# Performance work log

Hardware: AMD Instinct MI355X
Metric: run time of the kernel (lower is better)

The kernel has to match this reference:

```python
import jax, jax.numpy as jnp
import numpy as np

HEADS = 8
DIM_HEAD = 32
EPS = 1e-5


def _rel_index(h, w):
    # matches Attention._generate_relative_index (static, computed on host)
    coords = np.stack(np.meshgrid(np.arange(h), np.arange(w), indexing='ij')).reshape(2, -1)
    rel = coords[:, :, None] - coords[:, None, :]  # [2, n, n]
    rel[0] += h - 1
    rel[1] += w - 1
    rel[0] *= 2 * w - 1
    idx = rel.sum(0).reshape(-1)
    # torch.clamp(relative_index, 0, max_index) -- indices are already in range here
    return jnp.asarray(np.clip(idx, 0, (2 * h - 1) * (2 * w - 1) - 1))


def _layernorm(x, g, b):
    m = jnp.mean(x, axis=-1, keepdims=True)
    v = jnp.var(x, axis=-1, keepdims=True)
    return (x - m) * jax.lax.rsqrt(v + EPS) * g + b


def setup_inputs() -> dict:
    key = jax.random.key(0)
    ks = jax.random.split(key, 6)
    B, C, H, W = 64, 384, 16, 16
    inner = HEADS * DIM_HEAD  # 256
    hid = 4 * C               # 1536
    def nrm(k, shape, s=0.02):
        return jax.random.normal(k, shape, jnp.float32) * s
    return {
        'x': jax.random.normal(ks[0], (B, C, H, W), jnp.float32),
        'ln1_g': jnp.ones((C,), jnp.float32),
        'ln1_b': jnp.zeros((C,), jnp.float32),
        'w_qkv': nrm(ks[1], (C, 3 * inner)),
        'bias_table': nrm(ks[2], ((2 * H - 1) * (2 * W - 1), HEADS)),
        'w_out': nrm(ks[3], (inner, C)),
        'b_out': jnp.zeros((C,), jnp.float32),
        'ln2_g': jnp.ones((C,), jnp.float32),
        'ln2_b': jnp.zeros((C,), jnp.float32),
        'w_ff1': nrm(ks[4], (C, hid)),
        'b_ff1': jnp.zeros((hid,), jnp.float32),
        'w_ff2': nrm(ks[5], (hid, C)),
        'b_ff2': jnp.zeros((C,), jnp.float32),
    }


def reference(x, ln1_g, ln1_b, w_qkv, bias_table, w_out, b_out,
              ln2_g, ln2_b, w_ff1, b_ff1, w_ff2, b_ff2):
    B, C, H, W = x.shape
    n = H * W
    t = x.reshape(B, C, n).transpose(0, 2, 1)  # [B, n, C]

    # --- attention branch (PreNorm(LayerNorm) -> Attention) ---
    a = _layernorm(t, ln1_g, ln1_b)
    qkv = a @ w_qkv  # [B, n, 3*inner]
    q, k, v = jnp.split(qkv, 3, axis=-1)
    def split_heads(z):
        return z.reshape(B, n, HEADS, DIM_HEAD).transpose(0, 2, 1, 3)  # [B, h, n, d]
    q, k, v = split_heads(q), split_heads(k), split_heads(v)
    dots = jnp.einsum('bhid,bhjd->bhij', q, k) * (DIM_HEAD ** -0.5)
    idx = _rel_index(H, W)  # [n*n]
    rel_bias = bias_table[idx].reshape(n, n, HEADS).transpose(2, 0, 1)[None]  # [1, h, n, n]
    attn = jax.nn.softmax(dots + rel_bias, axis=-1)
    o = jnp.einsum('bhij,bhjd->bhid', attn, v)
    o = o.transpose(0, 2, 1, 3).reshape(B, n, HEADS * DIM_HEAD)
    attn_out = o @ w_out + b_out  # to_out Linear (dropout=0)

    # --- feedforward branch (PreNorm(LayerNorm) -> FFN) ---
    f = _layernorm(t, ln2_g, ln2_b)
    f = jax.nn.gelu(f @ w_ff1 + b_ff1, approximate=False) @ w_ff2 + b_ff2

    y = t + attn_out + f  # x_adjusted + attn_out + ff_out
    return y.transpose(0, 2, 1).reshape(B, C, H, W)
```

## Files before the change

### kernel.cpp

```cpp
#include <hip/hip_runtime.h>

typedef __bf16 bf16;
typedef __bf16 bf16x8 __attribute__((ext_vector_type(8)));
typedef float f32x4 __attribute__((ext_vector_type(4)));

__device__ __forceinline__ void gll16(const void* g, void* l) {
    __builtin_amdgcn_global_load_lds((const __attribute__((address_space(1))) void*)g,
                                     (__attribute__((address_space(3))) void*)l, 16, 0, 0);
}

#define WBAR(N) asm volatile("s_waitcnt vmcnt(" #N ")\n\ts_barrier" ::: "memory")

__device__ __forceinline__ float gelu_f(float v) {
    float x2 = v * v;
    float sn = v * fmaf(-0.0713540072f, x2, -1.5957691216f);
    float e  = __expf(sn);
    return v * __builtin_amdgcn_rcpf(1.0f + e);
}

__launch_bounds__(256)
__global__ void prep_kernel(const float* __restrict__ wqkv, const float* __restrict__ wout,
                            const float* __restrict__ wff1, const float* __restrict__ wff2,
                            bf16* __restrict__ wqkvT, bf16* __restrict__ woutT,
                            bf16* __restrict__ wff1T, bf16* __restrict__ wff2T,
                            const float* __restrict__ x,
                            const float* __restrict__ g1, const float* __restrict__ b1,
                            const float* __restrict__ g2, const float* __restrict__ b2,
                            bf16* __restrict__ a, bf16* __restrict__ f) {
    __shared__ __align__(16) float smem[12672 + 512 + 64];
    const int tid = threadIdx.x;
    int g = blockIdx.x;
    if (g < 1536) {
        float (*tl)[33] = (float (*)[33])smem;
        const float* in; bf16* out; int R, Cc, bx, by;
        if (g < 288)       { in = wqkv; out = wqkvT; R = 384;  Cc = 768;  bx = g % 24; by = g / 24; }
        else if (g < 384)  { g -= 288; in = wout; out = woutT; R = 256;  Cc = 384;  bx = g % 12; by = g / 12; }
        else if (g < 960)  { g -= 384; in = wff1; out = wff1T; R = 384;  Cc = 1536; bx = g % 48; by = g / 48; }
        else               { g -= 960; in = wff2; out = wff2T; R = 1536; Cc = 384;  bx = g % 12; by = g / 12; }
        const int c0 = bx * 32, r0 = by * 32;
        const int cl = tid & 31, r8 = tid >> 5;
#pragma unroll
        for (int k = 0; k < 4; k++) {
            int r = k * 8 + r8;
            tl[r][cl] = in[(size_t)(r0 + r) * Cc + c0 + cl];
        }
        __syncthreads();
#pragma unroll
        for (int k = 0; k < 4; k++) {
            int cc = k * 8 + r8;
            out[(size_t)(c0 + cc) * R + r0 + cl] = (bf16)tl[cl][cc];
        }
        return;
    }
    g -= 1536;
    float (*tile)[33] = (float (*)[33])smem;
    float (*S)[32]  = (float (*)[32])(smem + 12672);
    float (*SS)[32] = (float (*)[32])(smem + 12928);
    float* Mn = smem + 13184;
    float* Rs = smem + 13216;
    const int bb = g >> 3;
    const int i0 = (g & 7) * 32;
    {
        const int i_l = tid & 31, c_l = tid >> 5;
        const size_t base = (size_t)bb * 384 * 256 + i0 + i_l;
#pragma unroll 6
        for (int c = c_l; c < 384; c += 8)
            tile[c][i_l] = x[base + (size_t)c * 256];
    }
    __syncthreads();
    {
        const int i_s = tid & 31, p = tid >> 5;
        float s = 0.f, ss = 0.f;
#pragma unroll 6
        for (int j = 0; j < 48; j++) {
            float v = tile[p * 48 + j][i_s];
            s += v; ss += v * v;
        }
        S[p][i_s] = s; SS[p][i_s] = ss;
    }
    __syncthreads();
    if (tid < 32) {
        float t1 = 0.f, t2 = 0.f;
#pragma unroll
        for (int p = 0; p < 8; p++) { t1 += S[p][tid]; t2 += SS[p][tid]; }
        float mean = t1 * (1.0f / 384.0f);
        float var  = t2 * (1.0f / 384.0f) - mean * mean;
        Mn[tid] = mean;
        Rs[tid] = rsqrtf(var + 1e-5f);
    }
    __syncthreads();
    const int lane = tid & 63, w = tid >> 6;
#pragma unroll
    for (int rr = 0; rr < 8; rr++) {
        const int i = w * 8 + rr;
        const float mean = Mn[i], rstd = Rs[i];
        const size_t orow = ((size_t)bb * 256 + i0 + i) * 384;
#pragma unroll
        for (int pass = 0; pass < 6; pass++) {
            const int c = pass * 64 + lane;
            float nh = (tile[c][i] - mean) * rstd;
            a[orow + c] = (bf16)(nh * g1[c] + b1[c]);
            f[orow + c] = (bf16)(nh * g2[c] + b2[c]);
        }
    }
}

#define STAGE128(buf, kb)                                                   \
    {                                                                       \
        bf16* sA = lds + (buf) * 8192;                                      \
        bf16* sB = sA + 4096;                                               \
        gll16(Abase + (size_t)r0 * K + (kb) + ksw, sA + c0 * 8);            \
        gll16(Abase + (size_t)r1 * K + (kb) + ksw, sA + c1 * 8);            \
        gll16(Bbase + (size_t)r0 * K + (kb) + ksw, sB + c0 * 8);            \
        gll16(Bbase + (size_t)r1 * K + (kb) + ksw, sB + c1 * 8);            \
    }
#define COMPUTE128(buf)                                                     \
    {                                                                       \
        const bf16* sA = lds + (buf) * 8192;                                \
        const bf16* sB = sA + 4096;                                         \
        bf16x8 af[4], bfr[4];                                               \
        _Pragma("unroll") for (int i = 0; i < 4; i++)                       \
            af[i] = *(const bf16x8*)(sA + (wm + i * 16 + l16) * 32 + rsw);  \
        _Pragma("unroll") for (int j = 0; j < 4; j++)                       \
            bfr[j] = *(const bf16x8*)(sB + (wn + j * 16 + l16) * 32 + rsw); \
        _Pragma("unroll") for (int i = 0; i < 4; i++)                       \
            _Pragma("unroll") for (int j = 0; j < 4; j++)                   \
                acc[i][j] = __builtin_amdgcn_mfma_f32_16x16x32_bf16(af[i], bfr[j], acc[i][j], 0, 0, 0); \
    }
#define GEMM128_PRO_KLOOP(BID)                                                       \
    const int x_ = ((BID) >> 3) % nx;                                                \
    const int y_ = ((BID) & 7) + 8 * ((BID) / (8 * nx));                             \
    const int m0 = y_ * 128, n0 = x_ * 128;                                          \
    const int lane = tid & 63, w = tid >> 6;                                         \
    const int l16 = lane & 15, quad = lane >> 4;                                     \
    const int wm = (w & 1) * 64, wn = (w >> 1) * 64;                                 \
    f32x4 zero = {0.f, 0.f, 0.f, 0.f};                                               \
    f32x4 acc[4][4];                                                                 \
    _Pragma("unroll") for (int i = 0; i < 4; i++)                                    \
        _Pragma("unroll") for (int j = 0; j < 4; j++) acc[i][j] = zero;              \
    const int c0 = tid, c1 = tid + 256;                                              \
    const int r0 = c0 >> 2, r1 = c1 >> 2;                                            \
    const int ksw = (((tid & 3) ^ ((tid >> 3) & 3)) * 8);                            \
    const int rsw = ((quad ^ ((l16 >> 1) & 3)) * 8);                                 \
    const bf16* Abase = A + (size_t)m0 * K;                                          \
    const bf16* Bbase = Bt + (size_t)n0 * K;                                         \
    STAGE128(0, 0);                                                                  \
    STAGE128(1, 32);                                                                 \
    const int nt = K >> 5;                                                           \
    int t = 0;                                                                       \
    for (; t < nt - 2; ++t) {                                                        \
        WBAR(4);                                                                     \
        STAGE128((t + 2) % 3, (t + 2) * 32);                                         \
        COMPUTE128(t % 3);                                                           \
    }                                                                                \
    WBAR(4); COMPUTE128(t % 3); ++t;                                                 \
    WBAR(0); COMPUTE128(t % 3);                                                      \
    __syncthreads();

template <int EPI>
__launch_bounds__(256)
__global__ void gemm_bt(const bf16* __restrict__ A, const bf16* __restrict__ Bt,
                        const float* __restrict__ bias, bf16* __restrict__ C,
                        int M, int N, int K, int nx) {
    __shared__ __align__(16) bf16 lds[24576];
    const int tid = threadIdx.x;
    GEMM128_PRO_KLOOP(blockIdx.x)
#pragma unroll
    for (int j = 0; j < 4; j++) {
        const int col = wn + j * 16 + l16;
        float bv = 0.f;
        if (EPI >= 1) bv = bias[n0 + col];
#pragma unroll
        for (int i = 0; i < 4; i++) {
            const int row0 = wm + i * 16 + quad * 4;
#pragma unroll
            for (int r = 0; r < 4; r++) {
                float v = acc[i][j][r] + bv;
                if (EPI == 2) v = gelu_f(v);
                lds[(row0 + r) * 128 + col] = (bf16)v;
            }
        }
    }
    __syncthreads();
#pragma unroll
    for (int it = 0; it < 8; it++) {
        const int ch = tid + it * 256;
        const int row = ch >> 4, cc = (ch & 15) * 8;
        *(bf16x8*)(C + (size_t)(m0 + row) * N + n0 + cc) = *(const bf16x8*)(lds + row * 128 + cc);
    }
}

__launch_bounds__(256)
__global__ void stage3_kernel(const bf16* __restrict__ A, const bf16* __restrict__ Bt,
                              const float* __restrict__ bias, bf16* __restrict__ C,
                              const bf16* __restrict__ qkv, const float* __restrict__ btab,
                              bf16* __restrict__ o) {
    __shared__ __align__(16) char smem[70928];
    const int tid = threadIdx.x;
    const int gg = blockIdx.x;
    if (gg & 3) {
        const int bid = (gg >> 2) * 3 + (gg & 3) - 1;
        bf16* lds = (bf16*)smem;
        const int K = 384, N = 1536, nx = 12;
        GEMM128_PRO_KLOOP(bid)
#pragma unroll
        for (int j = 0; j < 4; j++) {
            const int col = wn + j * 16 + l16;
            const float bv = bias[n0 + col];
#pragma unroll
            for (int i = 0; i < 4; i++) {
                const int row0 = wm + i * 16 + quad * 4;
#pragma unroll
                for (int r = 0; r < 4; r++) {
                    float v = gelu_f(acc[i][j][r] + bv);
                    lds[(row0 + r) * 128 + col] = (bf16)v;
                }
            }
        }
        __syncthreads();
#pragma unroll
        for (int it = 0; it < 8; it++) {
            const int ch = tid + it * 256;
            const int row = ch >> 4, cc = (ch & 15) * 8;
            *(bf16x8*)(C + (size_t)(m0 + row) * N + n0 + cc) = *(const bf16x8*)(lds + row * 128 + cc);
        }
        return;
    }
    const int aid = gg >> 2;
    float* sbias = (float*)smem;
    bf16* sK = (bf16*)(smem + 3856);
    bf16 (*sVt)[264] = (bf16 (*)[264])(smem + 20240);
    bf16 (*sP)[16][264] = (bf16 (*)[16][264])(smem + 37136);
    const int h  = (aid >> 3) & 7;
    const int bb = (aid & 7) + 8 * (aid >> 6);
    const int lane = tid & 63, w = tid >> 6;
    const int l16 = lane & 15, quad = lane >> 4;
    const int rsw = ((quad ^ ((l16 >> 1) & 3)) * 8);
    const size_t qkvb = (size_t)bb * 256 * 768;
    const bf16* Qbase = qkv + qkvb + h * 32;
    const bf16* Kbase = qkv + qkvb + 256 + h * 32;
    const bf16* Vbase = qkv + qkvb + 512 + h * 32;

    for (int e = tid; e < 961; e += 256) sbias[e] = btab[e * 8 + h];
#pragma unroll
    for (int it = 0; it < 4; it++) {
        const int ch = it * 256 + tid;
        const int row = ch >> 2;
        const int d8 = (((ch & 3) ^ ((ch >> 3) & 3)) * 8);
        gll16(Kbase + (size_t)row * 768 + d8, sK + ch * 8);
    }
#pragma unroll
    for (int it = 0; it < 4; it++) {
        const int ch = it * 256 + tid;
        const int k = ch >> 2, d8 = (ch & 3) * 8;
        bf16x8 vv = *(const bf16x8*)(Vbase + (size_t)k * 768 + d8);
#pragma unroll
        for (int j = 0; j < 8; j++)
            sVt[d8 + j][k] = vv[j];
    }
    __syncthreads();

    f32x4 zero = {0.f, 0.f, 0.f, 0.f};
    for (int qc = 0; qc < 4; qc++) {
        const int qbase = qc * 64 + w * 16;
        bf16x8 qf = *(const bf16x8*)(Qbase + (size_t)(qbase + l16) * 768 + quad * 8);
        f32x4 s[16];
#pragma unroll
        for (int kt = 0; kt < 16; kt++) {
            bf16x8 kf = *(const bf16x8*)(sK + (kt * 16 + l16) * 32 + rsw);
            s[kt] = __builtin_amdgcn_mfma_f32_16x16x32_bf16(qf, kf, zero, 0, 0, 0);
        }
        const int qi0 = qbase + quad * 4;
        float mx[4] = {-1e30f, -1e30f, -1e30f, -1e30f};
#pragma unroll
        for (int kt = 0; kt < 16; kt++) {
            const int j = kt * 16 + l16;
            const int yj = j >> 4, xj = j & 15;
#pragma unroll
            for (int r = 0; r < 4; r++) {
                const int q = qi0 + r;
                const int tix = ((q >> 4) - yj + 15) * 31 + ((q & 15) - xj + 15);
                float v = s[kt][r] * 0.17677669529663687f + sbias[tix];
                s[kt][r] = v;
                mx[r] = fmaxf(mx[r], v);
            }
        }
#pragma unroll
        for (int r = 0; r < 4; r++)
            for (int msk = 1; msk < 16; msk <<= 1)
                mx[r] = fmaxf(mx[r], __shfl_xor(mx[r], msk, 64));
        float sum[4] = {0.f, 0.f, 0.f, 0.f};
#pragma unroll
        for (int kt = 0; kt < 16; kt++)
#pragma unroll
            for (int r = 0; r < 4; r++) {
                float e = __expf(s[kt][r] - mx[r]);
                s[kt][r] = e;
                sum[r] += e;
            }
#pragma unroll
        for (int r = 0; r < 4; r++) {
            for (int msk = 1; msk < 16; msk <<= 1)
                sum[r] += __shfl_xor(sum[r], msk, 64);
            sum[r] = 1.0f / sum[r];
        }
#pragma unroll
        for (int kt = 0; kt < 16; kt++)
#pragma unroll
            for (int r = 0; r < 4; r++)
                sP[w][quad * 4 + r][kt * 16 + l16] = (bf16)(s[kt][r] * sum[r]);
        f32x4 oacc[2];
        oacc[0] = zero; oacc[1] = zero;
#pragma unroll
        for (int ks = 0; ks < 8; ks++) {
            bf16x8 pf = *(const bf16x8*)(&sP[w][l16][ks * 32 + quad * 8]);
#pragma unroll
            for (int dt = 0; dt < 2; dt++) {
                bf16x8 vf = *(const bf16x8*)(&sVt[dt * 16 + l16][ks * 32 + quad * 8]);
                oacc[dt] = __builtin_amdgcn_mfma_f32_16x16x32_bf16(pf, vf, oacc[dt], 0, 0, 0);
            }
        }
#pragma unroll
        for (int dt = 0; dt < 2; dt++)
#pragma unroll
            for (int r = 0; r < 4; r++)
                o[(size_t)(bb * 256 + qbase + quad * 4 + r) * 256 + h * 32 + dt * 16 + l16] = (bf16)oacc[dt][r];
    }
}

__launch_bounds__(256)
__global__ void fin_dual(const bf16* __restrict__ Af, const bf16* __restrict__ Bf,
                         const bf16* __restrict__ Ao, const bf16* __restrict__ Bo,
                         const float* __restrict__ bff2, const float* __restrict__ bout,
                         const float* __restrict__ xres, float* __restrict__ out, int nx) {
    __shared__ __align__(16) bf16 lds[24576];
    const int tid = threadIdx.x;
    const int g = blockIdx.x;
    const int x_ = (g >> 3) % nx;
    const int y_ = (g & 7) + 8 * (g / (8 * nx));
    const int m0 = y_ * 128, n0 = x_ * 128;
    const int lane = tid & 63, w = tid >> 6;
    const int l16 = lane & 15, quad = lane >> 4;
    const int wm = (w & 1) * 64, wn = (w >> 1) * 64;
    f32x4 acc[4][4];
    { f32x4 z = {0.f, 0.f, 0.f, 0.f};
#pragma unroll
      for (int i = 0; i < 4; i++)
#pragma unroll
          for (int j = 0; j < 4; j++) acc[i][j] = z; }
    const int c0 = tid, c1 = tid + 256;
    const int r0 = c0 >> 2, r1 = c1 >> 2;
    const int ksw = (((tid & 3) ^ ((tid >> 3) & 3)) * 8);
    const int rsw = ((quad ^ ((l16 >> 1) & 3)) * 8);
    const bf16* A1 = Af + (size_t)m0 * 1536;
    const bf16* B1 = Bf + (size_t)n0 * 1536;
    const bf16* A2 = Ao + (size_t)m0 * 256;
    const bf16* B2 = Bo + (size_t)n0 * 256;

#define STGD(buf, s)                                                                \
    {   bf16* sA = lds + (buf) * 8192;                                              \
        bf16* sB = sA + 4096;                                                       \
        if ((s) < 48) {                                                             \
            const int kb = (s) * 32;                                                \
            gll16(A1 + (size_t)r0 * 1536 + kb + ksw, sA + c0 * 8);                  \
            gll16(A1 + (size_t)r1 * 1536 + kb + ksw, sA + c1 * 8);                  \
            gll16(B1 + (size_t)r0 * 1536 + kb + ksw, sB + c0 * 8);                  \
            gll16(B1 + (size_t)r1 * 1536 + kb + ksw, sB + c1 * 8);                  \
        } else {                                                                    \
            const int kb = ((s) - 48) * 32;                                         \
            gll16(A2 + (size_t)r0 * 256 + kb + ksw, sA + c0 * 8);                   \
            gll16(A2 + (size_t)r1 * 256 + kb + ksw, sA + c1 * 8);                   \
            gll16(B2 + (size_t)r0 * 256 + kb + ksw, sB + c0 * 8);                   \
            gll16(B2 + (size_t)r1 * 256 + kb + ksw, sB + c1 * 8);                   \
        } }

    STGD(0, 0); STGD(1, 1);
    int s = 0;
    for (; s < 54; ++s) {
        WBAR(4);
        STGD((s + 2) % 3, s + 2);
        COMPUTE128(s % 3);
    }
    WBAR(4); COMPUTE128(s % 3); ++s;
    WBAR(0); COMPUTE128(s % 3);
    __syncthreads();
#undef STGD

#pragma unroll
    for (int j = 0; j < 4; j++) {
        const int col = wn + j * 16 + l16;
        const float bv = bff2[n0 + col] + bout[n0 + col];
#pragma unroll
        for (int i = 0; i < 4; i++) {
            const int row0 = wm + i * 16 + quad * 4;
#pragma unroll
            for (int r = 0; r < 4; r++)
                lds[col * 132 + row0 + r] = (bf16)(acc[i][j][r] + bv);
        }
    }
    __syncthreads();
    const int b = m0 >> 8, ib = m0 & 255;
#pragma unroll
    for (int it = 0; it < 8; it++) {
        const int ch = tid + it * 256;
        const int cl = ch >> 4, ic = (ch & 15) * 8;
        const size_t base = (size_t)(b * 384 + n0 + cl) * 256 + ib + ic;
        bf16x8 ff = *(const bf16x8*)(lds + cl * 132 + ic);
        const f32x4* xr = (const f32x4*)(xres + base);
        f32x4 o0, o1;
#pragma unroll
        for (int e = 0; e < 4; e++) o0[e] = xr[0][e] + (float)ff[e];
#pragma unroll
        for (int e = 0; e < 4; e++) o1[e] = xr[1][e] + (float)ff[e + 4];
        ((f32x4*)(out + base))[0] = o0;
        ((f32x4*)(out + base))[1] = o1;
    }
}

extern "C" void kernel_launch(void* const* d_in, const int* in_sizes, int n_in,
                              void* d_out, int out_size, void* d_ws, size_t ws_size,
                              hipStream_t stream) {
    const float* x    = (const float*)d_in[0];
    const float* g1   = (const float*)d_in[1];
    const float* b1   = (const float*)d_in[2];
    const float* wqkv = (const float*)d_in[3];
    const float* btab = (const float*)d_in[4];
    const float* wout = (const float*)d_in[5];
    const float* bout = (const float*)d_in[6];
    const float* g2   = (const float*)d_in[7];
    const float* b2   = (const float*)d_in[8];
    const float* wff1 = (const float*)d_in[9];
    const float* bff1 = (const float*)d_in[10];
    const float* wff2 = (const float*)d_in[11];
    const float* bff2 = (const float*)d_in[12];
    float* out = (float*)d_out;

    bf16* ws = (bf16*)d_ws;
    const size_t NA = 6291456;
    bf16* wqkvT   = ws;
    bf16* woutT   = wqkvT + 294912;
    bf16* wff1T   = woutT + 98304;
    bf16* wff2T   = wff1T + 589824;
    bf16* f_buf   = ws + 1572864;
    bf16* a_buf   = f_buf + NA;
    bf16* qkv_buf = a_buf + NA;
    bf16* o_buf   = qkv_buf + 12582912;
    bf16* ffh_buf = o_buf + 4194304;

    dim3 b256(256);
    prep_kernel<<<2048, b256, 0, stream>>>(wqkv, wout, wff1, wff2, wqkvT, woutT, wff1T, wff2T,
                                           x, g1, b1, g2, b2, a_buf, f_buf);
    gemm_bt<0><<<6 * 128, b256, 0, stream>>>(a_buf, wqkvT, nullptr, qkv_buf, 16384, 768, 384, 6);
    stage3_kernel<<<2048, b256, 0, stream>>>(f_buf, wff1T, bff1, ffh_buf, qkv_buf, btab, o_buf);
    fin_dual<<<3 * 128, b256, 0, stream>>>(ffh_buf, wff2T, o_buf, woutT, bff2, bout, x, out, 3);
}
```

Baseline: 235.4 us.

## Split fused attention/FF1 kernel and use 128x256 GEMM tiles

Replaces the combined stage3 kernel, which interleaved attention blocks with FF1 GEMM blocks, with a standalone attention kernel followed by a separate FF1 GEMM launch. Both the QKV and FF1 GEMMs move to a new 128x256 tile kernel with 8 N-subtiles per wave, for more reuse of each A tile per K step. The change cuts block counts and raises the per-thread register and LDS footprint, which can lower occupancy. It also gives up the overlap of attention and GEMM work that the fused launch had.

```diff
diff --git a/kernel.cpp b/kernel.cpp
--- a/kernel.cpp
+++ b/kernel.cpp
@@ -105,15 +105,95 @@
     }
 }
 
-#define STAGE128(buf, kb)                                                   \
+#define STAGEW(buf, kb)                                                     \
     {                                                                       \
-        bf16* sA = lds + (buf) * 8192;                                      \
+        bf16* sA = lds + (buf) * 12288;                                     \
         bf16* sB = sA + 4096;                                               \
-        gll16(Abase + (size_t)r0 * K + (kb) + ksw, sA + c0 * 8);            \
-        gll16(Abase + (size_t)r1 * K + (kb) + ksw, sA + c1 * 8);            \
-        gll16(Bbase + (size_t)r0 * K + (kb) + ksw, sB + c0 * 8);            \
-        gll16(Bbase + (size_t)r1 * K + (kb) + ksw, sB + c1 * 8);            \
-    }
+        gll16(Abase + (size_t)rS * K + (kb) + ksw, sA + tid * 8);           \
+        gll16(Abase + (size_t)(rS + 64) * K + (kb) + ksw, sA + (tid + 256) * 8); \
+        gll16(Bbase + (size_t)rS * K + (kb) + ksw, sB + tid * 8);           \
+        gll16(Bbase + (size_t)(rS + 64) * K + (kb) + ksw, sB + (tid + 256) * 8); \
+        gll16(Bbase + (size_t)(rS + 128) * K + (kb) + ksw, sB + (tid + 512) * 8); \
+        gll16(Bbase + (size_t)(rS + 192) * K + (kb) + ksw, sB + (tid + 768) * 8); \
+    }
+#define COMPUTEW(buf)                                                       \
+    {                                                                       \
+        const bf16* sA = lds + (buf) * 12288;                               \
+        const bf16* sB = sA + 4096;                                         \
+        bf16x8 af[4], bfr[8];                                               \
+        _Pragma("unroll") for (int i = 0; i < 4; i++)                       \
+            af[i] = *(const bf16x8*)(sA + (wm + i * 16 + l16) * 32 + rsw);  \
+        _Pragma("unroll") for (int j = 0; j < 8; j++)                       \
+            bfr[j] = *(const bf16x8*)(sB + (wn + j * 16 + l16) * 32 + rsw); \
+        _Pragma("unroll") for (int i = 0; i < 4; i++)                       \
+            _Pragma("unroll") for (int j = 0; j < 8; j++)                   \
+                acc[i][j] = __builtin_amdgcn_mfma_f32_16x16x32_bf16(af[i], bfr[j], acc[i][j], 0, 0, 0); \
+    }
+
+template <int EPI>
+__launch_bounds__(256)
+__global__ void gemm_w(const bf16* __restrict__ A, const bf16* __restrict__ Bt,
+                       const float* __restrict__ bias, bf16* __restrict__ C,
+                       int M, int N, int K, int nx) {
+    __shared__ __align__(16) bf16 lds[36864];
+    const int tid = threadIdx.x;
+    const int g = blockIdx.x;
+    const int x_ = (g >> 3) % nx;
+    const int y_ = (g & 7) + 8 * (g / (8 * nx));
+    const int m0 = y_ * 128, n0 = x_ * 256;
+    const int lane = tid & 63, w = tid >> 6;
+    const int l16 = lane & 15, quad = lane >> 4;
+    const int wm = (w & 1) * 64, wn = (w >> 1) * 128;
+    f32x4 acc[4][8];
+    { f32x4 z = {0.f, 0.f, 0.f, 0.f};
+#pragma unroll
+      for (int i = 0; i < 4; i++)
+#pragma unroll
+          for (int j = 0; j < 8; j++) acc[i][j] = z; }
+    const int rS = tid >> 2;
+    const int ksw = (((tid & 3) ^ ((tid >> 3) & 3)) * 8);
+    const int rsw = ((quad ^ ((l16 >> 1) & 3)) * 8);
+    const bf16* Abase = A + (size_t)m0 * K;
+    const bf16* Bbase = Bt + (size_t)n0 * K;
+
+    STAGEW(0, 0);
+    STAGEW(1, 32);
+    const int nt = K >> 5;
+    int t = 0;
+    for (; t < nt - 2; ++t) {
+        WBAR(6);
+        STAGEW((t + 2) % 3, (t + 2) * 32);
+        COMPUTEW(t % 3);
+    }
+    WBAR(6); COMPUTEW(t % 3); ++t;
+    WBAR(0); COMPUTEW(t % 3);
+    __syncthreads();
+
+#pragma unroll
+    for (int j = 0; j < 8; j++) {
+        const int col = wn + j * 16 + l16;
+        float bv = 0.f;
+        if (EPI >= 1) bv = bias[n0 + col];
+#pragma unroll
+        for (int i = 0; i < 4; i++) {
+            const int row0 = wm + i * 16 + quad * 4;
+#pragma unroll
+            for (int r = 0; r < 4; r++) {
+                float v = acc[i][j][r] + bv;
+                if (EPI == 2) v = gelu_f(v);
+                lds[(row0 + r) * 256 + col] = (bf16)v;
+            }
+        }
+    }
+    __syncthreads();
+#pragma unroll
+    for (int it = 0; it < 16; it++) {
+        const int ch = tid + it * 256;
+        const int row = ch >> 5, cc = (ch & 31) * 8;
+        *(bf16x8*)(C + (size_t)(m0 + row) * N + n0 + cc) = *(const bf16x8*)(lds + row * 256 + cc);
+    }
+}
+
 #define COMPUTE128(buf)                                                     \
     {                                                                       \
         const bf16* sA = lds + (buf) * 8192;                                \
@@ -127,206 +207,6 @@
             _Pragma("unroll") for (int j = 0; j < 4; j++)                   \
                 acc[i][j] = __builtin_amdgcn_mfma_f32_16x16x32_bf16(af[i], bfr[j], acc[i][j], 0, 0, 0); \
     }
-#define GEMM128_PRO_KLOOP(BID)                                                       \
-    const int x_ = ((BID) >> 3) % nx;                                                \
-    const int y_ = ((BID) & 7) + 8 * ((BID) / (8 * nx));                             \
-    const int m0 = y_ * 128, n0 = x_ * 128;                                          \
-    const int lane = tid & 63, w = tid >> 6;                                         \
-    const int l16 = lane & 15, quad = lane >> 4;                                     \
-    const int wm = (w & 1) * 64, wn = (w >> 1) * 64;                                 \
-    f32x4 zero = {0.f, 0.f, 0.f, 0.f};                                               \
-    f32x4 acc[4][4];                                                                 \
-    _Pragma("unroll") for (int i = 0; i < 4; i++)                                    \
-        _Pragma("unroll") for (int j = 0; j < 4; j++) acc[i][j] = zero;              \
-    const int c0 = tid, c1 = tid + 256;                                              \
-    const int r0 = c0 >> 2, r1 = c1 >> 2;                                            \
-    const int ksw = (((tid & 3) ^ ((tid >> 3) & 3)) * 8);                            \
-    const int rsw = ((quad ^ ((l16 >> 1) & 3)) * 8);                                 \
-    const bf16* Abase = A + (size_t)m0 * K;                                          \
-    const bf16* Bbase = Bt + (size_t)n0 * K;                                         \
-    STAGE128(0, 0);                                                                  \
-    STAGE128(1, 32);                                                                 \
-    const int nt = K >> 5;                                                           \
-    int t = 0;                                                                       \
-    for (; t < nt - 2; ++t) {                                                        \
-        WBAR(4);                                                                     \
-        STAGE128((t + 2) % 3, (t + 2) * 32);                                         \
-        COMPUTE128(t % 3);                                                           \
-    }                                                                                \
-    WBAR(4); COMPUTE128(t % 3); ++t;                                                 \
-    WBAR(0); COMPUTE128(t % 3);                                                      \
-    __syncthreads();
-
-template <int EPI>
-__launch_bounds__(256)
-__global__ void gemm_bt(const bf16* __restrict__ A, const bf16* __restrict__ Bt,
-                        const float* __restrict__ bias, bf16* __restrict__ C,
-                        int M, int N, int K, int nx) {
-    __shared__ __align__(16) bf16 lds[24576];
-    const int tid = threadIdx.x;
-    GEMM128_PRO_KLOOP(blockIdx.x)
-#pragma unroll
-    for (int j = 0; j < 4; j++) {
-        const int col = wn + j * 16 + l16;
-        float bv = 0.f;
-        if (EPI >= 1) bv = bias[n0 + col];
-#pragma unroll
-        for (int i = 0; i < 4; i++) {
-            const int row0 = wm + i * 16 + quad * 4;
-#pragma unroll
-            for (int r = 0; r < 4; r++) {
-                float v = acc[i][j][r] + bv;
-                if (EPI == 2) v = gelu_f(v);
-                lds[(row0 + r) * 128 + col] = (bf16)v;
-            }
-        }
-    }
-    __syncthreads();
-#pragma unroll
-    for (int it = 0; it < 8; it++) {
-        const int ch = tid + it * 256;
-        const int row = ch >> 4, cc = (ch & 15) * 8;
-        *(bf16x8*)(C + (size_t)(m0 + row) * N + n0 + cc) = *(const bf16x8*)(lds + row * 128 + cc);
-    }
-}
-
-__launch_bounds__(256)
-__global__ void stage3_kernel(const bf16* __restrict__ A, const bf16* __restrict__ Bt,
-                              const float* __restrict__ bias, bf16* __restrict__ C,
-                              const bf16* __restrict__ qkv, const float* __restrict__ btab,
-                              bf16* __restrict__ o) {
-    __shared__ __align__(16) char smem[70928];
-    const int tid = threadIdx.x;
-    const int gg = blockIdx.x;
-    if (gg & 3) {
-        const int bid = (gg >> 2) * 3 + (gg & 3) - 1;
-        bf16* lds = (bf16*)smem;
-        const int K = 384, N = 1536, nx = 12;
-        GEMM128_PRO_KLOOP(bid)
-#pragma unroll
-        for (int j = 0; j < 4; j++) {
-            const int col = wn + j * 16 + l16;
-            const float bv = bias[n0 + col];
-#pragma unroll
-            for (int i = 0; i < 4; i++) {
-                const int row0 = wm + i * 16 + quad * 4;
-#pragma unroll
-                for (int r = 0; r < 4; r++) {
-                    float v = gelu_f(acc[i][j][r] + bv);
-                    lds[(row0 + r) * 128 + col] = (bf16)v;
-                }
-            }
-        }
-        __syncthreads();
-#pragma unroll
-        for (int it = 0; it < 8; it++) {
-            const int ch = tid + it * 256;
-            const int row = ch >> 4, cc = (ch & 15) * 8;
-            *(bf16x8*)(C + (size_t)(m0 + row) * N + n0 + cc) = *(const bf16x8*)(lds + row * 128 + cc);
-        }
-        return;
-    }
-    const int aid = gg >> 2;
-    float* sbias = (float*)smem;
-    bf16* sK = (bf16*)(smem + 3856);
-    bf16 (*sVt)[264] = (bf16 (*)[264])(smem + 20240);
-    bf16 (*sP)[16][264] = (bf16 (*)[16][264])(smem + 37136);
-    const int h  = (aid >> 3) & 7;
-    const int bb = (aid & 7) + 8 * (aid >> 6);
-    const int lane = tid & 63, w = tid >> 6;
-    const int l16 = lane & 15, quad = lane >> 4;
-    const int rsw = ((quad ^ ((l16 >> 1) & 3)) * 8);
-    const size_t qkvb = (size_t)bb * 256 * 768;
-    const bf16* Qbase = qkv + qkvb + h * 32;
-    const bf16* Kbase = qkv + qkvb + 256 + h * 32;
-    const bf16* Vbase = qkv + qkvb + 512 + h * 32;
-
-    for (int e = tid; e < 961; e += 256) sbias[e] = btab[e * 8 + h];
-#pragma unroll
-    for (int it = 0; it < 4; it++) {
-        const int ch = it * 256 + tid;
-        const int row = ch >> 2;
-        const int d8 = (((ch & 3) ^ ((ch >> 3) & 3)) * 8);
-        gll16(Kbase + (size_t)row * 768 + d8, sK + ch * 8);
-    }
-#pragma unroll
-    for (int it = 0; it < 4; it++) {
-        const int ch = it * 256 + tid;
-        const int k = ch >> 2, d8 = (ch & 3) * 8;
-        bf16x8 vv = *(const bf16x8*)(Vbase + (size_t)k * 768 + d8);
-#pragma unroll
-        for (int j = 0; j < 8; j++)
-            sVt[d8 + j][k] = vv[j];
-    }
-    __syncthreads();
-
-    f32x4 zero = {0.f, 0.f, 0.f, 0.f};
-    for (int qc = 0; qc < 4; qc++) {
-        const int qbase = qc * 64 + w * 16;
-        bf16x8 qf = *(const bf16x8*)(Qbase + (size_t)(qbase + l16) * 768 + quad * 8);
-        f32x4 s[16];
-#pragma unroll
-        for (int kt = 0; kt < 16; kt++) {
-            bf16x8 kf = *(const bf16x8*)(sK + (kt * 16 + l16) * 32 + rsw);
-            s[kt] = __builtin_amdgcn_mfma_f32_16x16x32_bf16(qf, kf, zero, 0, 0, 0);
-        }
-        const int qi0 = qbase + quad * 4;
-        float mx[4] = {-1e30f, -1e30f, -1e30f, -1e30f};
-#pragma unroll
-        for (int kt = 0; kt < 16; kt++) {
-            const int j = kt * 16 + l16;
-            const int yj = j >> 4, xj = j & 15;
-#pragma unroll
-            for (int r = 0; r < 4; r++) {
-                const int q = qi0 + r;
-                const int tix = ((q >> 4) - yj + 15) * 31 + ((q & 15) - xj + 15);
-                float v = s[kt][r] * 0.17677669529663687f + sbias[tix];
-                s[kt][r] = v;
-                mx[r] = fmaxf(mx[r], v);
-            }
-        }
-#pragma unroll
-        for (int r = 0; r < 4; r++)
-            for (int msk = 1; msk < 16; msk <<= 1)
-                mx[r] = fmaxf(mx[r], __shfl_xor(mx[r], msk, 64));
-        float sum[4] = {0.f, 0.f, 0.f, 0.f};
-#pragma unroll
-        for (int kt = 0; kt < 16; kt++)
-#pragma unroll
-            for (int r = 0; r < 4; r++) {
-                float e = __expf(s[kt][r] - mx[r]);
-                s[kt][r] = e;
-                sum[r] += e;
-            }
-#pragma unroll
-        for (int r = 0; r < 4; r++) {
-            for (int msk = 1; msk < 16; msk <<= 1)
-                sum[r] += __shfl_xor(sum[r], msk, 64);
-            sum[r] = 1.0f / sum[r];
-        }
-#pragma unroll
-        for (int kt = 0; kt < 16; kt++)
-#pragma unroll
-            for (int r = 0; r < 4; r++)
-                sP[w][quad * 4 + r][kt * 16 + l16] = (bf16)(s[kt][r] * sum[r]);
-        f32x4 oacc[2];
-        oacc[0] = zero; oacc[1] = zero;
-#pragma unroll
-        for (int ks = 0; ks < 8; ks++) {
-            bf16x8 pf = *(const bf16x8*)(&sP[w][l16][ks * 32 + quad * 8]);
-#pragma unroll
-            for (int dt = 0; dt < 2; dt++) {
-                bf16x8 vf = *(const bf16x8*)(&sVt[dt * 16 + l16][ks * 32 + quad * 8]);
-                oacc[dt] = __builtin_amdgcn_mfma_f32_16x16x32_bf16(pf, vf, oacc[dt], 0, 0, 0);
-            }
-        }
-#pragma unroll
-        for (int dt = 0; dt < 2; dt++)
-#pragma unroll
-            for (int r = 0; r < 4; r++)
-                o[(size_t)(bb * 256 + qbase + quad * 4 + r) * 256 + h * 32 + dt * 16 + l16] = (bf16)oacc[dt][r];
-    }
-}
 
 __launch_bounds__(256)
 __global__ void fin_dual(const bf16* __restrict__ Af, const bf16* __restrict__ Bf,
@@ -414,6 +294,113 @@
         for (int e = 0; e < 4; e++) o1[e] = xr[1][e] + (float)ff[e + 4];
         ((f32x4*)(out + base))[0] = o0;
         ((f32x4*)(out + base))[1] = o1;
+    }
+}
+
+__launch_bounds__(256)
+__global__ void attn_kernel(const bf16* __restrict__ qkv,
+                            const float* __restrict__ btab,
+                            bf16* __restrict__ o) {
+    __shared__ float sbias[961];
+    __shared__ __align__(16) bf16 sK[256 * 32];
+    __shared__ __align__(16) bf16 sVt[32][264];
+    __shared__ __align__(16) bf16 sP[4][16][264];
+    const int tid = threadIdx.x;
+    const int g = blockIdx.x;
+    const int h  = (g >> 3) & 7;
+    const int bb = (g & 7) + 8 * (g >> 6);
+    const int lane = tid & 63, w = tid >> 6;
+    const int l16 = lane & 15, quad = lane >> 4;
+    const int rsw = ((quad ^ ((l16 >> 1) & 3)) * 8);
+    const size_t qkvb = (size_t)bb * 256 * 768;
+    const bf16* Qbase = qkv + qkvb + h * 32;
+    const bf16* Kbase = qkv + qkvb + 256 + h * 32;
+    const bf16* Vbase = qkv + qkvb + 512 + h * 32;
+
+    for (int e = tid; e < 961; e += 256) sbias[e] = btab[e * 8 + h];
+#pragma unroll
+    for (int it = 0; it < 4; it++) {
+        const int ch = it * 256 + tid;
+        const int row = ch >> 2;
+        const int d8 = (((ch & 3) ^ ((ch >> 3) & 3)) * 8);
+        gll16(Kbase + (size_t)row * 768 + d8, sK + ch * 8);
+    }
+#pragma unroll
+    for (int it = 0; it < 4; it++) {
+        const int ch = it * 256 + tid;
+        const int k = ch >> 2, d8 = (ch & 3) * 8;
+        bf16x8 vv = *(const bf16x8*)(Vbase + (size_t)k * 768 + d8);
+#pragma unroll
+        for (int j = 0; j < 8; j++)
+            sVt[d8 + j][k] = vv[j];
+    }
+    __syncthreads();
+
+    f32x4 zero = {0.f, 0.f, 0.f, 0.f};
+    for (int qc = 0; qc < 4; qc++) {
+        const int qbase = qc * 64 + w * 16;
+        bf16x8 qf = *(const bf16x8*)(Qbase + (size_t)(qbase + l16) * 768 + quad * 8);
+        f32x4 s[16];
+#pragma unroll
+        for (int kt = 0; kt < 16; kt++) {
+            bf16x8 kf = *(const bf16x8*)(sK + (kt * 16 + l16) * 32 + rsw);
+            s[kt] = __builtin_amdgcn_mfma_f32_16x16x32_bf16(qf, kf, zero, 0, 0, 0);
+        }
+        const int qi0 = qbase + quad * 4;
+        float mx[4] = {-1e30f, -1e30f, -1e30f, -1e30f};
+#pragma unroll
+        for (int kt = 0; kt < 16; kt++) {
+            const int j = kt * 16 + l16;
+            const int yj = j >> 4, xj = j & 15;
+#pragma unroll
+            for (int r = 0; r < 4; r++) {
+                const int q = qi0 + r;
+                const int tix = ((q >> 4) - yj + 15) * 31 + ((q & 15) - xj + 15);
+                float v = s[kt][r] * 0.17677669529663687f + sbias[tix];
+                s[kt][r] = v;
+                mx[r] = fmaxf(mx[r], v);
+            }
+        }
+#pragma unroll
+        for (int r = 0; r < 4; r++)
+            for (int msk = 1; msk < 16; msk <<= 1)
+                mx[r] = fmaxf(mx[r], __shfl_xor(mx[r], msk, 64));
+        float sum[4] = {0.f, 0.f, 0.f, 0.f};
+#pragma unroll
+        for (int kt = 0; kt < 16; kt++)
+#pragma unroll
+            for (int r = 0; r < 4; r++) {
+                float e = __expf(s[kt][r] - mx[r]);
+                s[kt][r] = e;
+                sum[r] += e;
+            }
+#pragma unroll
+        for (int r = 0; r < 4; r++) {
+            for (int msk = 1; msk < 16; msk <<= 1)
+                sum[r] += __shfl_xor(sum[r], msk, 64);
+            sum[r] = 1.0f / sum[r];
+        }
+#pragma unroll
+        for (int kt = 0; kt < 16; kt++)
+#pragma unroll
+            for (int r = 0; r < 4; r++)
+                sP[w][quad * 4 + r][kt * 16 + l16] = (bf16)(s[kt][r] * sum[r]);
+        f32x4 oacc[2];
+        oacc[0] = zero; oacc[1] = zero;
+#pragma unroll
+        for (int ks = 0; ks < 8; ks++) {
+            bf16x8 pf = *(const bf16x8*)(&sP[w][l16][ks * 32 + quad * 8]);
+#pragma unroll
+            for (int dt = 0; dt < 2; dt++) {
+                bf16x8 vf = *(const bf16x8*)(&sVt[dt * 16 + l16][ks * 32 + quad * 8]);
+                oacc[dt] = __builtin_amdgcn_mfma_f32_16x16x32_bf16(pf, vf, oacc[dt], 0, 0, 0);
+            }
+        }
+#pragma unroll
+        for (int dt = 0; dt < 2; dt++)
+#pragma unroll
+            for (int r = 0; r < 4; r++)
+                o[(size_t)(bb * 256 + qbase + quad * 4 + r) * 256 + h * 32 + dt * 16 + l16] = (bf16)oacc[dt][r];
     }
 }
 
@@ -450,7 +437,8 @@
     dim3 b256(256);
     prep_kernel<<<2048, b256, 0, stream>>>(wqkv, wout, wff1, wff2, wqkvT, woutT, wff1T, wff2T,
                                            x, g1, b1, g2, b2, a_buf, f_buf);
-    gemm_bt<0><<<6 * 128, b256, 0, stream>>>(a_buf, wqkvT, nullptr, qkv_buf, 16384, 768, 384, 6);
-    stage3_kernel<<<2048, b256, 0, stream>>>(f_buf, wff1T, bff1, ffh_buf, qkv_buf, btab, o_buf);
+    gemm_w<0><<<3 * 128, b256, 0, stream>>>(a_buf, wqkvT, nullptr, qkv_buf, 16384, 768, 384, 3);
+    attn_kernel<<<512, b256, 0, stream>>>(qkv_buf, btab, o_buf);
+    gemm_w<2><<<6 * 128, b256, 0, stream>>>(f_buf, wff1T, bff1, ffh_buf, 16384, 1536, 384, 6);
     fin_dual<<<3 * 128, b256, 0, stream>>>(ffh_buf, wff2T, o_buf, woutT, bff2, bout, x, out, 3);
 }
```

Result: no change. 232.6 us (-1.2%).

## Split attention from FF1 GEMM, precompute expanded bias table, fold q scale

Applied to the files above, without the earlier changes.

The combined stage3 kernel, which interleaved attention blocks with FF1 GEMM blocks, is split into a standalone attention kernel and a separate gemm_bt<2> launch. The relative position bias is expanded once in prep_kernel into a dense transposed [h, j, q] float table, so attention reads a vectorized f32x4 bias instead of gathering from LDS with index arithmetic. The softmax scale is folded into the Q columns in the QKV GEMM epilogue. The trade is an extra launch, a serial dependency between two kernels that previously overlapped, and 2 MB of extra bias traffic read from global memory.

```diff
diff --git a/kernel.cpp b/kernel.cpp
--- a/kernel.cpp
+++ b/kernel.cpp
@@ -26,7 +26,8 @@
                             const float* __restrict__ x,
                             const float* __restrict__ g1, const float* __restrict__ b1,
                             const float* __restrict__ g2, const float* __restrict__ b2,
-                            bf16* __restrict__ a, bf16* __restrict__ f) {
+                            bf16* __restrict__ a, bf16* __restrict__ f,
+                            const float* __restrict__ btab, float* __restrict__ biasT) {
     __shared__ __align__(16) float smem[12672 + 512 + 64];
     const int tid = threadIdx.x;
     int g = blockIdx.x;
@@ -49,6 +50,19 @@
         for (int k = 0; k < 4; k++) {
             int cc = k * 8 + r8;
             out[(size_t)(c0 + cc) * R + r0 + cl] = (bf16)tl[cl][cc];
+        }
+        return;
+    }
+    if (g >= 2048) {
+        const int gb = g - 2048;
+        const int h = gb >> 6;
+        const int j0 = (gb & 63) * 4;
+        const int q = tid;
+#pragma unroll
+        for (int jj = 0; jj < 4; jj++) {
+            const int j = j0 + jj;
+            const int tix = ((q >> 4) - (j >> 4) + 15) * 31 + ((q & 15) - (j & 15) + 15);
+            biasT[((size_t)(h * 256 + j) << 8) + q] = btab[tix * 8 + h];
         }
         return;
     }
@@ -165,18 +179,20 @@
     __shared__ __align__(16) bf16 lds[24576];
     const int tid = threadIdx.x;
     GEMM128_PRO_KLOOP(blockIdx.x)
+    const float qsc = (EPI == 3 && n0 < 256) ? 0.17677669529663687f : 1.0f;
 #pragma unroll
     for (int j = 0; j < 4; j++) {
         const int col = wn + j * 16 + l16;
         float bv = 0.f;
-        if (EPI >= 1) bv = bias[n0 + col];
+        if (EPI == 2) bv = bias[n0 + col];
 #pragma unroll
         for (int i = 0; i < 4; i++) {
             const int row0 = wm + i * 16 + quad * 4;
 #pragma unroll
             for (int r = 0; r < 4; r++) {
-                float v = acc[i][j][r] + bv;
-                if (EPI == 2) v = gelu_f(v);
+                float v = acc[i][j][r];
+                if (EPI == 3) v *= qsc;
+                if (EPI == 2) v = gelu_f(v + bv);
                 lds[(row0 + r) * 128 + col] = (bf16)v;
             }
         }
@@ -187,144 +203,6 @@
         const int ch = tid + it * 256;
         const int row = ch >> 4, cc = (ch & 15) * 8;
         *(bf16x8*)(C + (size_t)(m0 + row) * N + n0 + cc) = *(const bf16x8*)(lds + row * 128 + cc);
-    }
-}
-
-__launch_bounds__(256)
-__global__ void stage3_kernel(const bf16* __restrict__ A, const bf16* __restrict__ Bt,
-                              const float* __restrict__ bias, bf16* __restrict__ C,
-                              const bf16* __restrict__ qkv, const float* __restrict__ btab,
-                              bf16* __restrict__ o) {
-    __shared__ __align__(16) char smem[70928];
-    const int tid = threadIdx.x;
-    const int gg = blockIdx.x;
-    if (gg & 3) {
-        const int bid = (gg >> 2) * 3 + (gg & 3) - 1;
-        bf16* lds = (bf16*)smem;
-        const int K = 384, N = 1536, nx = 12;
-        GEMM128_PRO_KLOOP(bid)
-#pragma unroll
-        for (int j = 0; j < 4; j++) {
-            const int col = wn + j * 16 + l16;
-            const float bv = bias[n0 + col];
-#pragma unroll
-            for (int i = 0; i < 4; i++) {
-                const int row0 = wm + i * 16 + quad * 4;
-#pragma unroll
-                for (int r = 0; r < 4; r++) {
-                    float v = gelu_f(acc[i][j][r] + bv);
-                    lds[(row0 + r) * 128 + col] = (bf16)v;
-                }
-            }
-        }
-        __syncthreads();
-#pragma unroll
-        for (int it = 0; it < 8; it++) {
-            const int ch = tid + it * 256;
-            const int row = ch >> 4, cc = (ch & 15) * 8;
-            *(bf16x8*)(C + (size_t)(m0 + row) * N + n0 + cc) = *(const bf16x8*)(lds + row * 128 + cc);
-        }
-        return;
-    }
-    const int aid = gg >> 2;
-    float* sbias = (float*)smem;
-    bf16* sK = (bf16*)(smem + 3856);
-    bf16 (*sVt)[264] = (bf16 (*)[264])(smem + 20240);
-    bf16 (*sP)[16][264] = (bf16 (*)[16][264])(smem + 37136);
-    const int h  = (aid >> 3) & 7;
-    const int bb = (aid & 7) + 8 * (aid >> 6);
-    const int lane = tid & 63, w = tid >> 6;
-    const int l16 = lane & 15, quad = lane >> 4;
-    const int rsw = ((quad ^ ((l16 >> 1) & 3)) * 8);
-    const size_t qkvb = (size_t)bb * 256 * 768;
-    const bf16* Qbase = qkv + qkvb + h * 32;
-    const bf16* Kbase = qkv + qkvb + 256 + h * 32;
-    const bf16* Vbase = qkv + qkvb + 512 + h * 32;
-
-    for (int e = tid; e < 961; e += 256) sbias[e] = btab[e * 8 + h];
-#pragma unroll
-    for (int it = 0; it < 4; it++) {
-        const int ch = it * 256 + tid;
-        const int row = ch >> 2;
-        const int d8 = (((ch & 3) ^ ((ch >> 3) & 3)) * 8);
-        gll16(Kbase + (size_t)row * 768 + d8, sK + ch * 8);
-    }
-#pragma unroll
-    for (int it = 0; it < 4; it++) {
-        const int ch = it * 256 + tid;
-        const int k = ch >> 2, d8 = (ch & 3) * 8;
-        bf16x8 vv = *(const bf16x8*)(Vbase + (size_t)k * 768 + d8);
-#pragma unroll
-        for (int j = 0; j < 8; j++)
-            sVt[d8 + j][k] = vv[j];
-    }
-    __syncthreads();
-
-    f32x4 zero = {0.f, 0.f, 0.f, 0.f};
-    for (int qc = 0; qc < 4; qc++) {
-        const int qbase = qc * 64 + w * 16;
-        bf16x8 qf = *(const bf16x8*)(Qbase + (size_t)(qbase + l16) * 768 + quad * 8);
-        f32x4 s[16];
-#pragma unroll
-        for (int kt = 0; kt < 16; kt++) {
-            bf16x8 kf = *(const bf16x8*)(sK + (kt * 16 + l16) * 32 + rsw);
-            s[kt] = __builtin_amdgcn_mfma_f32_16x16x32_bf16(qf, kf, zero, 0, 0, 0);
-        }
-        const int qi0 = qbase + quad * 4;
-        float mx[4] = {-1e30f, -1e30f, -1e30f, -1e30f};
-#pragma unroll
-        for (int kt = 0; kt < 16; kt++) {
-            const int j = kt * 16 + l16;
-            const int yj = j >> 4, xj = j & 15;
-#pragma unroll
-            for (int r = 0; r < 4; r++) {
-                const int q = qi0 + r;
-                const int tix = ((q >> 4) - yj + 15) * 31 + ((q & 15) - xj + 15);
-                float v = s[kt][r] * 0.17677669529663687f + sbias[tix];
-                s[kt][r] = v;
-                mx[r] = fmaxf(mx[r], v);
-            }
-        }
-#pragma unroll
-        for (int r = 0; r < 4; r++)
-            for (int msk = 1; msk < 16; msk <<= 1)
-                mx[r] = fmaxf(mx[r], __shfl_xor(mx[r], msk, 64));
-        float sum[4] = {0.f, 0.f, 0.f, 0.f};
-#pragma unroll
-        for (int kt = 0; kt < 16; kt++)
-#pragma unroll
-            for (int r = 0; r < 4; r++) {
-                float e = __expf(s[kt][r] - mx[r]);
-                s[kt][r] = e;
-                sum[r] += e;
-            }
-#pragma unroll
-        for (int r = 0; r < 4; r++) {
-            for (int msk = 1; msk < 16; msk <<= 1)
-                sum[r] += __shfl_xor(sum[r], msk, 64);
-            sum[r] = 1.0f / sum[r];
-        }
-#pragma unroll
-        for (int kt = 0; kt < 16; kt++)
-#pragma unroll
-            for (int r = 0; r < 4; r++)
-                sP[w][quad * 4 + r][kt * 16 + l16] = (bf16)(s[kt][r] * sum[r]);
-        f32x4 oacc[2];
-        oacc[0] = zero; oacc[1] = zero;
-#pragma unroll
-        for (int ks = 0; ks < 8; ks++) {
-            bf16x8 pf = *(const bf16x8*)(&sP[w][l16][ks * 32 + quad * 8]);
-#pragma unroll
-            for (int dt = 0; dt < 2; dt++) {
-                bf16x8 vf = *(const bf16x8*)(&sVt[dt * 16 + l16][ks * 32 + quad * 8]);
-                oacc[dt] = __builtin_amdgcn_mfma_f32_16x16x32_bf16(pf, vf, oacc[dt], 0, 0, 0);
-            }
-        }
-#pragma unroll
-        for (int dt = 0; dt < 2; dt++)
-#pragma unroll
-            for (int r = 0; r < 4; r++)
-                o[(size_t)(bb * 256 + qbase + quad * 4 + r) * 256 + h * 32 + dt * 16 + l16] = (bf16)oacc[dt][r];
     }
 }
 
@@ -414,6 +292,109 @@
         for (int e = 0; e < 4; e++) o1[e] = xr[1][e] + (float)ff[e + 4];
         ((f32x4*)(out + base))[0] = o0;
         ((f32x4*)(out + base))[1] = o1;
+    }
+}
+
+__launch_bounds__(256)
+__global__ void attn_kernel(const bf16* __restrict__ qkv,
+                            const float* __restrict__ biasT,
+                            bf16* __restrict__ o) {
+    __shared__ __align__(16) bf16 sK[256 * 32];
+    __shared__ __align__(16) bf16 sVt[32][264];
+    __shared__ __align__(16) bf16 sP[4][16][264];
+    const int tid = threadIdx.x;
+    const int g = blockIdx.x;
+    const int h  = (g >> 3) & 7;
+    const int bb = (g & 7) + 8 * (g >> 6);
+    const int lane = tid & 63, w = tid >> 6;
+    const int l16 = lane & 15, quad = lane >> 4;
+    const int rsw = ((quad ^ ((l16 >> 1) & 3)) * 8);
+    const size_t qkvb = (size_t)bb * 256 * 768;
+    const bf16* Qbase = qkv + qkvb + h * 32;
+    const bf16* Kbase = qkv + qkvb + 256 + h * 32;
+    const bf16* Vbase = qkv + qkvb + 512 + h * 32;
+    const float* bT = biasT + ((size_t)h << 16);
+
+#pragma unroll
+    for (int it = 0; it < 4; it++) {
+        const int ch = it * 256 + tid;
+        const int row = ch >> 2;
+        const int d8 = (((ch & 3) ^ ((ch >> 3) & 3)) * 8);
+        gll16(Kbase + (size_t)row * 768 + d8, sK + ch * 8);
+    }
+#pragma unroll
+    for (int it = 0; it < 4; it++) {
+        const int ch = it * 256 + tid;
+        const int k = ch >> 2, d8 = (ch & 3) * 8;
+        bf16x8 vv = *(const bf16x8*)(Vbase + (size_t)k * 768 + d8);
+#pragma unroll
+        for (int j = 0; j < 8; j++)
+            sVt[d8 + j][k] = vv[j];
+    }
+    __syncthreads();
+
+    f32x4 zero = {0.f, 0.f, 0.f, 0.f};
+    for (int qc = 0; qc < 4; qc++) {
+        const int qbase = qc * 64 + w * 16;
+        bf16x8 qf = *(const bf16x8*)(Qbase + (size_t)(qbase + l16) * 768 + quad * 8);
+        const int qi0 = qbase + quad * 4;
+        f32x4 s[16];
+#pragma unroll
+        for (int kt = 0; kt < 16; kt++) {
+            bf16x8 kf = *(const bf16x8*)(sK + (kt * 16 + l16) * 32 + rsw);
+            s[kt] = __builtin_amdgcn_mfma_f32_16x16x32_bf16(qf, kf, zero, 0, 0, 0);
+        }
+        float mx[4] = {-1e30f, -1e30f, -1e30f, -1e30f};
+#pragma unroll
+        for (int kt = 0; kt < 16; kt++) {
+            const f32x4 bv = *(const f32x4*)(bT + ((kt * 16 + l16) << 8) + qi0);
+#pragma unroll
+            for (int r = 0; r < 4; r++) {
+                float v = s[kt][r] + bv[r];
+                s[kt][r] = v;
+                mx[r] = fmaxf(mx[r], v);
+            }
+        }
+#pragma unroll
+        for (int r = 0; r < 4; r++)
+            for (int msk = 1; msk < 16; msk <<= 1)
+                mx[r] = fmaxf(mx[r], __shfl_xor(mx[r], msk, 64));
+        float sum[4] = {0.f, 0.f, 0.f, 0.f};
+#pragma unroll
+        for (int kt = 0; kt < 16; kt++)
+#pragma unroll
+            for (int r = 0; r < 4; r++) {
+                float e = __expf(s[kt][r] - mx[r]);
+                s[kt][r] = e;
+                sum[r] += e;
+            }
+#pragma unroll
+        for (int r = 0; r < 4; r++) {
+            for (int msk = 1; msk < 16; msk <<= 1)
+                sum[r] += __shfl_xor(sum[r], msk, 64);
+            sum[r] = 1.0f / sum[r];
+        }
+#pragma unroll
+        for (int kt = 0; kt < 16; kt++)
+#pragma unroll
+            for (int r = 0; r < 4; r++)
+                sP[w][quad * 4 + r][kt * 16 + l16] = (bf16)(s[kt][r] * sum[r]);
+        f32x4 oacc[2];
+        oacc[0] = zero; oacc[1] = zero;
+#pragma unroll
+        for (int ks = 0; ks < 8; ks++) {
+            bf16x8 pf = *(const bf16x8*)(&sP[w][l16][ks * 32 + quad * 8]);
+#pragma unroll
+            for (int dt = 0; dt < 2; dt++) {
+                bf16x8 vf = *(const bf16x8*)(&sVt[dt * 16 + l16][ks * 32 + quad * 8]);
+                oacc[dt] = __builtin_amdgcn_mfma_f32_16x16x32_bf16(pf, vf, oacc[dt], 0, 0, 0);
+            }
+        }
+#pragma unroll
+        for (int dt = 0; dt < 2; dt++)
+#pragma unroll
+            for (int r = 0; r < 4; r++)
+                o[(size_t)(bb * 256 + qbase + quad * 4 + r) * 256 + h * 32 + dt * 16 + l16] = (bf16)oacc[dt][r];
     }
 }
 
@@ -446,11 +427,13 @@
     bf16* qkv_buf = a_buf + NA;
     bf16* o_buf   = qkv_buf + 12582912;
     bf16* ffh_buf = o_buf + 4194304;
+    float* biasT  = (float*)(ws + 56098816);
 
     dim3 b256(256);
-    prep_kernel<<<2048, b256, 0, stream>>>(wqkv, wout, wff1, wff2, wqkvT, woutT, wff1T, wff2T,
-                                           x, g1, b1, g2, b2, a_buf, f_buf);
-    gemm_bt<0><<<6 * 128, b256, 0, stream>>>(a_buf, wqkvT, nullptr, qkv_buf, 16384, 768, 384, 6);
-    stage3_kernel<<<2048, b256, 0, stream>>>(f_buf, wff1T, bff1, ffh_buf, qkv_buf, btab, o_buf);
+    prep_kernel<<<2560, b256, 0, stream>>>(wqkv, wout, wff1, wff2, wqkvT, woutT, wff1T, wff2T,
+                                           x, g1, b1, g2, b2, a_buf, f_buf, btab, biasT);
+    gemm_bt<3><<<6 * 128, b256, 0, stream>>>(a_buf, wqkvT, nullptr, qkv_buf, 16384, 768, 384, 6);
+    attn_kernel<<<512, b256, 0, stream>>>(qkv_buf, biasT, o_buf);
+    gemm_bt<2><<<12 * 128, b256, 0, stream>>>(f_buf, wff1T, bff1, ffh_buf, 16384, 1536, 384, 12);
     fin_dual<<<3 * 128, b256, 0, stream>>>(ffh_buf, wff2T, o_buf, woutT, bff2, bout, x, out, 3);
 }
```

Result: no change. 231.9 us (-1.5%).
